# Kernel optimization log

Hardware: AMD Instinct MI355X
Metric: run time of the kernel (lower is better)

The kernel has to match this reference:

```python
import jax, jax.numpy as jnp
import numpy as np


def setup_inputs() -> dict:
    key = jax.random.key(0)
    ks = jax.random.split(key, 8)
    B, T, DIM = 4096, 64, 16
    H1, H2, LAT = 256, 256, 64
    KD = DIM + LAT  # Koopman dim = 80
    x = jax.random.normal(ks[0], (B, T, DIM), dtype=jnp.float32)
    # Encoder: Linear(16->256, bias), Linear(256->256, bias), Linear(256->64, no bias)
    W1 = jax.random.normal(ks[1], (H1, DIM), dtype=jnp.float32) / np.sqrt(DIM)
    b1 = jnp.zeros((H1,), dtype=jnp.float32)
    W2 = jax.random.normal(ks[2], (H2, H1), dtype=jnp.float32) / np.sqrt(H1)
    b2 = jnp.zeros((H2,), dtype=jnp.float32)
    W3 = jax.random.normal(ks[3], (LAT, H2), dtype=jnp.float32) / np.sqrt(H2)
    # Koopman operator, scaled for stable 63-step rollout
    K = jax.random.normal(ks[4], (KD, KD), dtype=jnp.float32) * (0.9 / np.sqrt(KD))
    return {"x": x, "W1": W1, "b1": b1, "W2": W2, "b2": b2, "W3": W3,
            "K": K, "n_shifts": 64}


def reference(x, W1, b1, W2, b2, W3, K, n_shifts):
    # x: [B, T, dim]; slice to n_shifts steps
    x = x[:, :n_shifts, :]
    # Encoder MLP (relu on all but last layer; last layer bias-free, dropout p=0)
    h = jax.nn.relu(jnp.einsum('btd,hd->bth', x, W1) + b1)
    h = jax.nn.relu(jnp.einsum('bth,gh->btg', h, W2) + b2)
    g = jnp.einsum('btg,lg->btl', h, W3)
    y = jnp.concatenate([x, g], axis=-1)  # [B, T, dim+lat]
    # Linear recurrence: y_{n+1} = y_n @ K^T, starting from y[:, 0]
    y0 = y[:, 0, :]  # [B, KD]

    def step(carry, _):
        nxt = carry @ K.T
        return nxt, nxt

    _, rest = jax.lax.scan(step, y0, None, length=n_shifts - 1)  # [T-1, B, KD]
    y_pred = jnp.concatenate([y0[:, None, :], jnp.swapaxes(rest, 0, 1)], axis=1)
    return y, y_pred
```

## Files before the change

kernel.cpp:

```cpp
#include <hip/hip_runtime.h>
#include <hip/hip_bf16.h>

#define NB   4096
#define NT   64
#define NDIM 16
#define NH1  256
#define NH2  256
#define NLAT 64
#define NKD  80
#define YROW (NT * NKD)
#define KTAB 98304
#define KSLOT 15360
#define Y0F   1081344
#define HPLANE 393216

#define FROW 184
#define FIMG_B (80 * FROW * 2)

typedef __attribute__((ext_vector_type(8))) short bf16x8;
typedef __attribute__((ext_vector_type(4))) float f32x4;

#define MFMA __builtin_amdgcn_mfma_f32_16x16x32_bf16

static __device__ __forceinline__ short f2bf(float f) {
  __hip_bfloat16 b = __float2bfloat16(f);
  return __builtin_bit_cast(short, b);
}
static __device__ __forceinline__ float bf2f(short h) {
  union { unsigned u; float f; } v; v.u = ((unsigned)(unsigned short)h) << 16;
  return v.f;
}
static __device__ __forceinline__ bf16x8 pack8(float4 a, float4 b) {
  bf16x8 r;
  r[0] = f2bf(a.x); r[1] = f2bf(a.y); r[2] = f2bf(a.z); r[3] = f2bf(a.w);
  r[4] = f2bf(b.x); r[5] = f2bf(b.y); r[6] = f2bf(b.z); r[7] = f2bf(b.w);
  return r;
}

__global__ __launch_bounds__(256) void prep_kernel(const float* __restrict__ W1,
                                                   const float* __restrict__ W2,
                                                   const float* __restrict__ W3,
                                                   short* __restrict__ ws) {
  int i = blockIdx.x * 256 + threadIdx.x;
  {
    int e = i & 7, l = (i >> 3) & 63, nt = (i >> 9) & 15, kk = i >> 13;
    int g = nt * 16 + (l & 15);
    int h = kk * 32 + (l >> 4) * 8 + e;
    ws[i] = f2bf(W2[g * NH1 + h]);
  }
  if (i < 16384) {
    int e = i & 7, l = (i >> 3) & 63, nt = (i >> 9) & 3, kk = i >> 11;
    int g = nt * 16 + (l & 15);
    int h = kk * 32 + (l >> 4) * 8 + e;
    ws[65536 + i] = f2bf(W3[g * NH2 + h]);
  }
  if (i < 8192) {
    int e = i & 7, l = (i >> 3) & 63, nt = i >> 9;
    int g = nt * 16 + (l & 15);
    int k = (l >> 4) * 8 + e;
    ws[81920 + i] = (k < NDIM) ? f2bf(W1[g * NDIM + k]) : (short)0;
  }
}

template <int XSTRIDE, int MODE>
static __device__ __forceinline__ void mlp_body(long b, const float* __restrict__ x,
                                                const float* __restrict__ b1g,
                                                const float* __restrict__ b2g,
                                                const short* __restrict__ ws,
                                                float* __restrict__ yo,
                                                short* __restrict__ y0f,
                                                short* h1s, int tid) {
  const int lane = tid & 63;
  const int w    = tid >> 6;
  const int l15  = lane & 15;
  const int kg   = lane >> 4;

  const short* W2f = ws;
  const short* W3f = ws + 65536;
  const short* W1f = ws + 81920;

  const float4 xv =
      *(const float4*)(x + (b * 64 + (tid >> 2)) * XSTRIDE + (tid & 3) * 4);

  bf16x8 xf[4];
#pragma unroll
  for (int j = 0; j < 4; ++j) {
    const int tok = j * 16 + l15;
    bf16x8 f = {};
    if (kg < 2) {
      const float4* p = (const float4*)(x + (b * 64 + tok) * XSTRIDE + kg * 8);
      f = pack8(p[0], p[1]);
    }
    xf[j] = f;
  }

#pragma unroll
  for (int i = 0; i < 4; ++i) {
    const int mt = w * 4 + i;
    const bf16x8 wa = *(const bf16x8*)(W1f + (mt * 64 + lane) * 8);
    const float4 bias = *(const float4*)(b1g + mt * 16 + kg * 4);
#pragma unroll
    for (int j = 0; j < 4; ++j) {
      f32x4 c = {0.f, 0.f, 0.f, 0.f};
      c = MFMA(wa, xf[j], c, 0, 0, 0);
      const int tok = j * 16 + l15;
      float v0 = c[0] + bias.x; v0 = v0 > 0.f ? v0 : 0.f;
      float v1 = c[1] + bias.y; v1 = v1 > 0.f ? v1 : 0.f;
      float v2 = c[2] + bias.z; v2 = v2 > 0.f ? v2 : 0.f;
      float v3 = c[3] + bias.w; v3 = v3 > 0.f ? v3 : 0.f;
      short4 st = {f2bf(v0), f2bf(v1), f2bf(v2), f2bf(v3)};
      *(short4*)(h1s + tok * 264 + mt * 16 + kg * 4) = st;
    }
  }
  __syncthreads();

  f32x4 acc2[4][4];
#pragma unroll
  for (int i = 0; i < 4; ++i)
#pragma unroll
    for (int j = 0; j < 4; ++j) acc2[i][j] = (f32x4){0.f, 0.f, 0.f, 0.f};

#pragma unroll 2
  for (int kk = 0; kk < 8; ++kk) {
    bf16x8 wa[4], hb[4];
#pragma unroll
    for (int i = 0; i < 4; ++i)
      wa[i] = *(const bf16x8*)(W2f + ((kk * 16 + w * 4 + i) * 64 + lane) * 8);
#pragma unroll
    for (int j = 0; j < 4; ++j)
      hb[j] = *(const bf16x8*)(h1s + (j * 16 + l15) * 264 + kk * 32 + kg * 8);
#pragma unroll
    for (int i = 0; i < 4; ++i)
#pragma unroll
      for (int j = 0; j < 4; ++j)
        acc2[i][j] = MFMA(wa[i], hb[j], acc2[i][j], 0, 0, 0);
  }
  __syncthreads();

#pragma unroll
  for (int i = 0; i < 4; ++i) {
    const int mt = w * 4 + i;
    const float4 bias = *(const float4*)(b2g + mt * 16 + kg * 4);
#pragma unroll
    for (int j = 0; j < 4; ++j) {
      const int tok = j * 16 + l15;
      float v0 = acc2[i][j][0] + bias.x; v0 = v0 > 0.f ? v0 : 0.f;
      float v1 = acc2[i][j][1] + bias.y; v1 = v1 > 0.f ? v1 : 0.f;
      float v2 = acc2[i][j][2] + bias.z; v2 = v2 > 0.f ? v2 : 0.f;
      float v3 = acc2[i][j][3] + bias.w; v3 = v3 > 0.f ? v3 : 0.f;
      short4 st = {f2bf(v0), f2bf(v1), f2bf(v2), f2bf(v3)};
      *(short4*)(h1s + tok * 264 + mt * 16 + kg * 4) = st;
    }
  }
  __syncthreads();

  f32x4 acc3[4];
#pragma unroll
  for (int j = 0; j < 4; ++j) acc3[j] = (f32x4){0.f, 0.f, 0.f, 0.f};
#pragma unroll 2
  for (int kk = 0; kk < 8; ++kk) {
    const bf16x8 wa = *(const bf16x8*)(W3f + ((kk * 4 + w) * 64 + lane) * 8);
#pragma unroll
    for (int j = 0; j < 4; ++j) {
      const bf16x8 hb =
          *(const bf16x8*)(h1s + (j * 16 + l15) * 264 + kk * 32 + kg * 8);
      acc3[j] = MFMA(wa, hb, acc3[j], 0, 0, 0);
    }
  }

  if (MODE == 0) {
    *(float4*)(yo + (b * 64 + (tid >> 2)) * 80 + (tid & 3) * 4) = xv;
#pragma unroll
    for (int j = 0; j < 4; ++j) {
      const int tok = j * 16 + l15;
      *(float4*)(yo + (b * 64 + tok) * 80 + 16 + w * 16 + kg * 4) =
          *(float4*)&acc3[j];
    }
  } else {
    {
      const int t0 = tid >> 2;
      const int gmt = (int)b * 4 + (t0 >> 4);
      const int c0x = (tid & 3) * 4;
      const int lanef = (c0x >> 3) * 16 + (t0 & 15);
      short h0 = f2bf(xv.x), h1 = f2bf(xv.y), h2 = f2bf(xv.z), h3 = f2bf(xv.w);
      short4 hs = {h0, h1, h2, h3};
      short4 ls = {f2bf(xv.x - bf2f(h0)), f2bf(xv.y - bf2f(h1)),
                   f2bf(xv.z - bf2f(h2)), f2bf(xv.w - bf2f(h3))};
      const int idx = ((gmt * 3 + 0) * 64 + lanef) * 8 + (c0x & 7);
      *(short4*)(y0f + idx) = hs;
      *(short4*)(y0f + HPLANE + idx) = ls;
    }
    const int c0 = 16 + w * 16 + kg * 4;
    const int kkf = c0 >> 5;
    const int lanef = ((c0 & 31) >> 3) * 16 + l15;
#pragma unroll
    for (int j = 0; j < 4; ++j) {
      const int gmt = (int)b * 4 + j;
      short h0 = f2bf(acc3[j][0]), h1 = f2bf(acc3[j][1]);
      short h2 = f2bf(acc3[j][2]), h3 = f2bf(acc3[j][3]);
      short4 hs = {h0, h1, h2, h3};
      short4 ls = {f2bf(acc3[j][0] - bf2f(h0)), f2bf(acc3[j][1] - bf2f(h1)),
                   f2bf(acc3[j][2] - bf2f(h2)), f2bf(acc3[j][3] - bf2f(h3))};
      const int idx = ((gmt * 3 + kkf) * 64 + lanef) * 8 + (c0 & 7);
      *(short4*)(y0f + idx) = hs;
      *(short4*)(y0f + HPLANE + idx) = ls;
    }
    {
      const int plane = tid & 1;
      const int lz = 32 + ((tid >> 1) & 31);
      const int gmt = (int)b * 4 + (tid >> 6);
      bf16x8 z = {};
      *(bf16x8*)(y0f + plane * HPLANE + ((gmt * 3 + 2) * 64 + lz) * 8) = z;
    }
  }
}

__global__ __launch_bounds__(256, 4) void kpow_mlp0_kernel(const float* __restrict__ Kg,
                                                           const float* __restrict__ x,
                                                           const float* __restrict__ b1g,
                                                           const float* __restrict__ b2g,
                                                           short* __restrict__ ws) {
  extern __shared__ char smem[];
  const int tid = threadIdx.x;

  if (blockIdx.x >= 63) {
    mlp_body<1024, 1>((long)(blockIdx.x - 63), x, b1g, b2g, ws, nullptr,
                      ws + Y0F, (short*)smem, tid);
    return;
  }

  short* kA   = (short*)smem;
  short* curA = (short*)(smem + FIMG_B);
  short* curB = (short*)(smem + 2 * FIMG_B);
  short* nxtA = (short*)(smem + 3 * FIMG_B);
  short* nxtB = (short*)(smem + 4 * FIMG_B);

  const int lane = tid & 63;
  const int w    = tid >> 6;
  const int l15  = lane & 15;
  const int kg   = lane >> 4;
  const int t    = blockIdx.x + 1;

  for (int i = tid; i < 6400; i += 256) {
    float v = Kg[i];
    int r = i / 80, c = i - r * 80;
    short hi = f2bf(v);
    short lo = f2bf(v - bf2f(hi));
    kA[r * FROW + c] = hi;        kA[r * FROW + 96 + c] = lo;
    curA[r * FROW + c] = hi;      curA[r * FROW + 96 + c] = lo;
    curB[c * FROW + r] = hi;      curB[c * FROW + 96 + r] = lo;
  }
  __syncthreads();

  auto mm = [&](const short* Ai, const short* Bi, short* DA, short* DB) {
    for (int id = w; id < 25; id += 4) {
      const int mt = id / 5, nt = id % 5;
      f32x4 acc = {0.f, 0.f, 0.f, 0.f};
#pragma unroll
      for (int kk = 0; kk < 3; ++kk) {
        const int k0 = kk * 32 + kg * 8;
        bf16x8 ah = {}, al = {}, bh = {}, bl = {};
        if (k0 < 80) {
          const short* ap = Ai + (mt * 16 + l15) * FROW + k0;
          const short* bp = Bi + (nt * 16 + l15) * FROW + k0;
          ah = *(const bf16x8*)ap;  al = *(const bf16x8*)(ap + 96);
          bh = *(const bf16x8*)bp;  bl = *(const bf16x8*)(bp + 96);
        }
        acc = MFMA(ah, bh, acc, 0, 0, 0);
        acc = MFMA(al, bh, acc, 0, 0, 0);
        acc = MFMA(ah, bl, acc, 0, 0, 0);
      }
      const int n = nt * 16 + l15;
      const int rowb = mt * 16 + kg * 4;
      short4 hs, ls;
#pragma unroll
      for (int r = 0; r < 4; ++r) {
        float v = acc[r];
        short hi = f2bf(v);
        short lo = f2bf(v - bf2f(hi));
        DA[(rowb + r) * FROW + n] = hi;
        DA[(rowb + r) * FROW + 96 + n] = lo;
        ((short*)&hs)[r] = hi;
        ((short*)&ls)[r] = lo;
      }
      *(short4*)(DB + n * FROW + rowb) = hs;
      *(short4*)(DB + n * FROW + 96 + rowb) = ls;
    }
    __syncthreads();
  };

  const int h = 31 - __clz(t);
  for (int bit = h - 1; bit >= 0; --bit) {
    mm(curA, curB, nxtA, nxtB);
    { short* p;
      p = curA; curA = nxtA; nxtA = p;
      p = curB; curB = nxtB; nxtB = p; }
    if ((t >> bit) & 1) {
      mm(kA, curB, nxtA, nxtB);
      { short* p;
        p = curA; curA = nxtA; nxtA = p;
        p = curB; curB = nxtB; nxtB = p; }
    }
  }

  short* kt = ws + KTAB + t * KSLOT;
  for (int s = tid; s < 960; s += 256) {
    int f = s >> 6, ln = s & 63;
    int kk = f / 5, nt = f % 5;
    int k0 = kk * 32 + (ln >> 4) * 8;
    int n  = nt * 16 + (ln & 15);
    bf16x8 h8 = {}, l8 = {};
    if (k0 < 80) {
      const short* ap = curA + n * FROW + k0;
      h8 = *(const bf16x8*)ap;
      l8 = *(const bf16x8*)(ap + 96);
    }
    *(bf16x8*)(kt + f * 512 + ln * 8) = h8;
    *(bf16x8*)(kt + 7680 + f * 512 + ln * 8) = l8;
  }
}

static __device__ __forceinline__ void ypred_body(int g, const short* __restrict__ ws,
                                                  float* __restrict__ yp, int tid) {
  const int lane = tid & 63;
  const int w    = tid >> 6;
  const int m16  = lane & 15;
  const int kg   = lane >> 4;
  const int bc   = g & 31;
  const int t    = g >> 5;
  const long b0  = (long)bc * 128;
  const short* y0f = ws + Y0F;

  if (t == 0) {
    for (int i = tid; i < 10240; i += 256) {
      const int r = i / 80, c = i - (i / 80) * 80;
      const int gmt = bc * 8 + (r >> 4);
      const int idx = ((gmt * 3 + (c >> 5)) * 64 + ((c & 31) >> 3) * 16 + (r & 15)) * 8 + (c & 7);
      yp[(b0 + r) * YROW + c] = bf2f(y0f[idx]) + bf2f(y0f[HPLANE + idx]);
    }
    return;
  }

  bf16x8 ah[2][3], al[2][3];
#pragma unroll
  for (int m = 0; m < 2; ++m) {
    const int gmt = bc * 8 + 2 * w + m;
#pragma unroll
    for (int kk = 0; kk < 3; ++kk) {
      const int idx = ((gmt * 3 + kk) * 64 + lane) * 8;
      ah[m][kk] = *(const bf16x8*)(y0f + idx);
      al[m][kk] = *(const bf16x8*)(y0f + HPLANE + idx);
    }
  }

  const short* kt = ws + KTAB + t * KSLOT;
  f32x4 acc[2][5];
#pragma unroll
  for (int m = 0; m < 2; ++m)
#pragma unroll
    for (int nt = 0; nt < 5; ++nt) acc[m][nt] = (f32x4){0.f, 0.f, 0.f, 0.f};

#pragma unroll
  for (int kk = 0; kk < 3; ++kk) {
#pragma unroll
    for (int nt = 0; nt < 5; ++nt) {
      const bf16x8 bh = *(const bf16x8*)(kt + ((kk * 5 + nt) * 64 + lane) * 8);
      const bf16x8 bl = *(const bf16x8*)(kt + 7680 + ((kk * 5 + nt) * 64 + lane) * 8);
#pragma unroll
      for (int m = 0; m < 2; ++m) {
        acc[m][nt] = MFMA(ah[m][kk], bh, acc[m][nt], 0, 0, 0);
        acc[m][nt] = MFMA(al[m][kk], bh, acc[m][nt], 0, 0, 0);
        acc[m][nt] = MFMA(ah[m][kk], bl, acc[m][nt], 0, 0, 0);
      }
    }
  }
#pragma unroll
  for (int m = 0; m < 2; ++m)
#pragma unroll
    for (int nt = 0; nt < 5; ++nt)
#pragma unroll
      for (int r = 0; r < 4; ++r)
        yp[(b0 + (2 * w + m) * 16 + kg * 4 + r) * YROW + (long)t * 80 + nt * 16 + m16] =
            acc[m][nt][r];
}

__global__ __launch_bounds__(256, 4) void fused_kernel(const float* __restrict__ x,
                                                       const float* __restrict__ b1g,
                                                       const float* __restrict__ b2g,
                                                       const short* __restrict__ ws,
                                                       float* __restrict__ y,
                                                       float* __restrict__ yp) {
  extern __shared__ char smem[];
  const int bid = blockIdx.x;
  const int g = bid / 3;
  const int r = bid - 3 * g;
  if (r == 2) {
    ypred_body(g, ws, yp, threadIdx.x);
  } else {
    mlp_body<16, 0>((long)(g * 2 + r), x, b1g, b2g, ws, y, nullptr,
                    (short*)smem, threadIdx.x);
  }
}

extern "C" void kernel_launch(void* const* d_in, const int* in_sizes, int n_in,
                              void* d_out, int out_size, void* d_ws, size_t ws_size,
                              hipStream_t stream) {
  const float* x  = (const float*)d_in[0];
  const float* W1 = (const float*)d_in[1];
  const float* b1 = (const float*)d_in[2];
  const float* W2 = (const float*)d_in[3];
  const float* b2 = (const float*)d_in[4];
  const float* W3 = (const float*)d_in[5];
  const float* Kg = (const float*)d_in[6];
  float* y  = (float*)d_out;
  float* yp = y + (long)NB * YROW;
  short* ws = (short*)d_ws;

  prep_kernel<<<256, 256, 0, stream>>>(W1, W2, W3, ws);
  kpow_mlp0_kernel<<<127, 256, 5 * FIMG_B, stream>>>(Kg, x, b1, b2, ws);
  fused_kernel<<<6144, 256, 64 * 264 * 2, stream>>>(x, b1, b2, ws, y, yp);
}
```

Measured before the change: 116.8 us.

## Split fused kernel into larger-tile MLP kernel and separate ypred kernel

Replaces the interleaved fused kernel, which ran 64-token MLP blocks alongside ypred blocks, with two launches. The first is a 512-thread MLP kernel that processes 256 tokens per block, reusing each loaded W2 fragment across 16 token tiles and prefetching the next W2 slice. The second is a standalone ypred kernel. The goal is to cut repeated weight fetches per token and raise MFMA density. The cost is an extra kernel launch, losing the overlap of MLP and ypred work, and a larger LDS footprint (about 135 KB) that may limit occupancy.

```diff
diff --git a/kernel.cpp b/kernel.cpp
--- a/kernel.cpp
+++ b/kernel.cpp
@@ -62,14 +62,12 @@
   }
 }
 
-template <int XSTRIDE, int MODE>
-static __device__ __forceinline__ void mlp_body(long b, const float* __restrict__ x,
-                                                const float* __restrict__ b1g,
-                                                const float* __restrict__ b2g,
-                                                const short* __restrict__ ws,
-                                                float* __restrict__ yo,
-                                                short* __restrict__ y0f,
-                                                short* h1s, int tid) {
+static __device__ __forceinline__ void mlp0_body(long b, const float* __restrict__ x,
+                                                 const float* __restrict__ b1g,
+                                                 const float* __restrict__ b2g,
+                                                 const short* __restrict__ ws,
+                                                 short* __restrict__ y0f,
+                                                 short* h1s, int tid) {
   const int lane = tid & 63;
   const int w    = tid >> 6;
   const int l15  = lane & 15;
@@ -80,7 +78,7 @@
   const short* W1f = ws + 81920;
 
   const float4 xv =
-      *(const float4*)(x + (b * 64 + (tid >> 2)) * XSTRIDE + (tid & 3) * 4);
+      *(const float4*)(x + (b * 64 + (tid >> 2)) * 1024 + (tid & 3) * 4);
 
   bf16x8 xf[4];
 #pragma unroll
@@ -88,7 +86,7 @@
     const int tok = j * 16 + l15;
     bf16x8 f = {};
     if (kg < 2) {
-      const float4* p = (const float4*)(x + (b * 64 + tok) * XSTRIDE + kg * 8);
+      const float4* p = (const float4*)(x + (b * 64 + tok) * 1024 + kg * 8);
       f = pack8(p[0], p[1]);
     }
     xf[j] = f;
@@ -168,50 +166,40 @@
     }
   }
 
-  if (MODE == 0) {
-    *(float4*)(yo + (b * 64 + (tid >> 2)) * 80 + (tid & 3) * 4) = xv;
-#pragma unroll
-    for (int j = 0; j < 4; ++j) {
-      const int tok = j * 16 + l15;
-      *(float4*)(yo + (b * 64 + tok) * 80 + 16 + w * 16 + kg * 4) =
-          *(float4*)&acc3[j];
-    }
-  } else {
-    {
-      const int t0 = tid >> 2;
-      const int gmt = (int)b * 4 + (t0 >> 4);
-      const int c0x = (tid & 3) * 4;
-      const int lanef = (c0x >> 3) * 16 + (t0 & 15);
-      short h0 = f2bf(xv.x), h1 = f2bf(xv.y), h2 = f2bf(xv.z), h3 = f2bf(xv.w);
-      short4 hs = {h0, h1, h2, h3};
-      short4 ls = {f2bf(xv.x - bf2f(h0)), f2bf(xv.y - bf2f(h1)),
-                   f2bf(xv.z - bf2f(h2)), f2bf(xv.w - bf2f(h3))};
-      const int idx = ((gmt * 3 + 0) * 64 + lanef) * 8 + (c0x & 7);
-      *(short4*)(y0f + idx) = hs;
-      *(short4*)(y0f + HPLANE + idx) = ls;
-    }
-    const int c0 = 16 + w * 16 + kg * 4;
-    const int kkf = c0 >> 5;
-    const int lanef = ((c0 & 31) >> 3) * 16 + l15;
-#pragma unroll
-    for (int j = 0; j < 4; ++j) {
-      const int gmt = (int)b * 4 + j;
-      short h0 = f2bf(acc3[j][0]), h1 = f2bf(acc3[j][1]);
-      short h2 = f2bf(acc3[j][2]), h3 = f2bf(acc3[j][3]);
-      short4 hs = {h0, h1, h2, h3};
-      short4 ls = {f2bf(acc3[j][0] - bf2f(h0)), f2bf(acc3[j][1] - bf2f(h1)),
-                   f2bf(acc3[j][2] - bf2f(h2)), f2bf(acc3[j][3] - bf2f(h3))};
-      const int idx = ((gmt * 3 + kkf) * 64 + lanef) * 8 + (c0 & 7);
-      *(short4*)(y0f + idx) = hs;
-      *(short4*)(y0f + HPLANE + idx) = ls;
-    }
-    {
-      const int plane = tid & 1;
-      const int lz = 32 + ((tid >> 1) & 31);
-      const int gmt = (int)b * 4 + (tid >> 6);
-      bf16x8 z = {};
-      *(bf16x8*)(y0f + plane * HPLANE + ((gmt * 3 + 2) * 64 + lz) * 8) = z;
-    }
+  {
+    const int t0 = tid >> 2;
+    const int gmt = (int)b * 4 + (t0 >> 4);
+    const int c0x = (tid & 3) * 4;
+    const int lanef = (c0x >> 3) * 16 + (t0 & 15);
+    short h0 = f2bf(xv.x), h1 = f2bf(xv.y), h2 = f2bf(xv.z), h3 = f2bf(xv.w);
+    short4 hs = {h0, h1, h2, h3};
+    short4 ls = {f2bf(xv.x - bf2f(h0)), f2bf(xv.y - bf2f(h1)),
+                 f2bf(xv.z - bf2f(h2)), f2bf(xv.w - bf2f(h3))};
+    const int idx = ((gmt * 3 + 0) * 64 + lanef) * 8 + (c0x & 7);
+    *(short4*)(y0f + idx) = hs;
+    *(short4*)(y0f + HPLANE + idx) = ls;
+  }
+  const int c0 = 16 + w * 16 + kg * 4;
+  const int kkf = c0 >> 5;
+  const int lanef = ((c0 & 31) >> 3) * 16 + l15;
+#pragma unroll
+  for (int j = 0; j < 4; ++j) {
+    const int gmt = (int)b * 4 + j;
+    short h0 = f2bf(acc3[j][0]), h1 = f2bf(acc3[j][1]);
+    short h2 = f2bf(acc3[j][2]), h3 = f2bf(acc3[j][3]);
+    short4 hs = {h0, h1, h2, h3};
+    short4 ls = {f2bf(acc3[j][0] - bf2f(h0)), f2bf(acc3[j][1] - bf2f(h1)),
+                 f2bf(acc3[j][2] - bf2f(h2)), f2bf(acc3[j][3] - bf2f(h3))};
+    const int idx = ((gmt * 3 + kkf) * 64 + lanef) * 8 + (c0 & 7);
+    *(short4*)(y0f + idx) = hs;
+    *(short4*)(y0f + HPLANE + idx) = ls;
+  }
+  {
+    const int plane = tid & 1;
+    const int lz = 32 + ((tid >> 1) & 31);
+    const int gmt = (int)b * 4 + (tid >> 6);
+    bf16x8 z = {};
+    *(bf16x8*)(y0f + plane * HPLANE + ((gmt * 3 + 2) * 64 + lz) * 8) = z;
   }
 }
 
@@ -224,8 +212,7 @@
   const int tid = threadIdx.x;
 
   if (blockIdx.x >= 63) {
-    mlp_body<1024, 1>((long)(blockIdx.x - 63), x, b1g, b2g, ws, nullptr,
-                      ws + Y0F, (short*)smem, tid);
+    mlp0_body((long)(blockIdx.x - 63), x, b1g, b2g, ws, ws + Y0F, (short*)smem, tid);
     return;
   }
 
@@ -320,14 +307,151 @@
   }
 }
 
-static __device__ __forceinline__ void ypred_body(int g, const short* __restrict__ ws,
-                                                  float* __restrict__ yp, int tid) {
+__global__ __launch_bounds__(512, 2) void mlp256_kernel(const float* __restrict__ x,
+                                                        const float* __restrict__ b1g,
+                                                        const float* __restrict__ b2g,
+                                                        const short* __restrict__ ws,
+                                                        float* __restrict__ y) {
+  extern __shared__ char smem[];
+  short* h1s = (short*)smem;
+
+  const int tid  = threadIdx.x;
+  const int lane = tid & 63;
+  const int w    = tid >> 6;
+  const int l15  = lane & 15;
+  const int kg   = lane >> 4;
+  const long b   = blockIdx.x;
+
+  const short* W2f = ws;
+  const short* W3f = ws + 65536;
+  const short* W1f = ws + 81920;
+
+#pragma unroll
+  for (int i = 0; i < 2; ++i) {
+    const int idx = i * 512 + tid;
+    const int tok = idx >> 2, c = (idx & 3) * 4;
+    const float4 v = *(const float4*)(x + (b * 256 + tok) * 16 + c);
+    *(float4*)(y + (b * 256 + tok) * 80 + c) = v;
+  }
+
+  {
+    const bf16x8 wa0 = *(const bf16x8*)(W1f + ((2 * w) * 64 + lane) * 8);
+    const bf16x8 wa1 = *(const bf16x8*)(W1f + ((2 * w + 1) * 64 + lane) * 8);
+    const float4 bias0 = *(const float4*)(b1g + (2 * w) * 16 + kg * 4);
+    const float4 bias1 = *(const float4*)(b1g + (2 * w + 1) * 16 + kg * 4);
+#pragma unroll
+    for (int nt = 0; nt < 16; ++nt) {
+      const int tok = nt * 16 + l15;
+      bf16x8 xf = {};
+      if (kg < 2) {
+        const float4* p = (const float4*)(x + (b * 256 + tok) * 16 + kg * 8);
+        xf = pack8(p[0], p[1]);
+      }
+      f32x4 c0 = {0.f, 0.f, 0.f, 0.f}, c1 = {0.f, 0.f, 0.f, 0.f};
+      c0 = MFMA(wa0, xf, c0, 0, 0, 0);
+      c1 = MFMA(wa1, xf, c1, 0, 0, 0);
+      float u0 = c0[0] + bias0.x; u0 = u0 > 0.f ? u0 : 0.f;
+      float u1 = c0[1] + bias0.y; u1 = u1 > 0.f ? u1 : 0.f;
+      float u2 = c0[2] + bias0.z; u2 = u2 > 0.f ? u2 : 0.f;
+      float u3 = c0[3] + bias0.w; u3 = u3 > 0.f ? u3 : 0.f;
+      short4 s0 = {f2bf(u0), f2bf(u1), f2bf(u2), f2bf(u3)};
+      *(short4*)(h1s + tok * 264 + (2 * w) * 16 + kg * 4) = s0;
+      float v0 = c1[0] + bias1.x; v0 = v0 > 0.f ? v0 : 0.f;
+      float v1 = c1[1] + bias1.y; v1 = v1 > 0.f ? v1 : 0.f;
+      float v2 = c1[2] + bias1.z; v2 = v2 > 0.f ? v2 : 0.f;
+      float v3 = c1[3] + bias1.w; v3 = v3 > 0.f ? v3 : 0.f;
+      short4 s1 = {f2bf(v0), f2bf(v1), f2bf(v2), f2bf(v3)};
+      *(short4*)(h1s + tok * 264 + (2 * w + 1) * 16 + kg * 4) = s1;
+    }
+  }
+  __syncthreads();
+
+  f32x4 acc2[2][16];
+#pragma unroll
+  for (int i = 0; i < 2; ++i)
+#pragma unroll
+    for (int j = 0; j < 16; ++j) acc2[i][j] = (f32x4){0.f, 0.f, 0.f, 0.f};
+
+  bf16x8 wa0 = *(const bf16x8*)(W2f + ((2 * w) * 64 + lane) * 8);
+  bf16x8 wa1 = *(const bf16x8*)(W2f + ((2 * w + 1) * 64 + lane) * 8);
+  for (int kk = 0; kk < 8; ++kk) {
+    bf16x8 nwa0, nwa1;
+    if (kk < 7) {
+      const short* wb = W2f + (((kk + 1) * 16 + 2 * w) * 64 + lane) * 8;
+      nwa0 = *(const bf16x8*)wb;
+      nwa1 = *(const bf16x8*)(wb + 512);
+    }
+#pragma unroll
+    for (int g = 0; g < 4; ++g) {
+      bf16x8 hb[4];
+#pragma unroll
+      for (int j = 0; j < 4; ++j)
+        hb[j] = *(const bf16x8*)(h1s + ((g * 4 + j) * 16 + l15) * 264 + kk * 32 + kg * 8);
+#pragma unroll
+      for (int j = 0; j < 4; ++j) {
+        acc2[0][g * 4 + j] = MFMA(wa0, hb[j], acc2[0][g * 4 + j], 0, 0, 0);
+        acc2[1][g * 4 + j] = MFMA(wa1, hb[j], acc2[1][g * 4 + j], 0, 0, 0);
+      }
+    }
+    wa0 = nwa0; wa1 = nwa1;
+  }
+  __syncthreads();
+
+  {
+    const float4 bias0 = *(const float4*)(b2g + (2 * w) * 16 + kg * 4);
+    const float4 bias1 = *(const float4*)(b2g + (2 * w + 1) * 16 + kg * 4);
+#pragma unroll
+    for (int j = 0; j < 16; ++j) {
+      const int tok = j * 16 + l15;
+      float u0 = acc2[0][j][0] + bias0.x; u0 = u0 > 0.f ? u0 : 0.f;
+      float u1 = acc2[0][j][1] + bias0.y; u1 = u1 > 0.f ? u1 : 0.f;
+      float u2 = acc2[0][j][2] + bias0.z; u2 = u2 > 0.f ? u2 : 0.f;
+      float u3 = acc2[0][j][3] + bias0.w; u3 = u3 > 0.f ? u3 : 0.f;
+      short4 s0 = {f2bf(u0), f2bf(u1), f2bf(u2), f2bf(u3)};
+      *(short4*)(h1s + tok * 264 + (2 * w) * 16 + kg * 4) = s0;
+      float v0 = acc2[1][j][0] + bias1.x; v0 = v0 > 0.f ? v0 : 0.f;
+      float v1 = acc2[1][j][1] + bias1.y; v1 = v1 > 0.f ? v1 : 0.f;
+      float v2 = acc2[1][j][2] + bias1.z; v2 = v2 > 0.f ? v2 : 0.f;
+      float v3 = acc2[1][j][3] + bias1.w; v3 = v3 > 0.f ? v3 : 0.f;
+      short4 s1 = {f2bf(v0), f2bf(v1), f2bf(v2), f2bf(v3)};
+      *(short4*)(h1s + tok * 264 + (2 * w + 1) * 16 + kg * 4) = s1;
+    }
+  }
+  __syncthreads();
+
+  const int mt3 = w & 3;
+  const int nh  = w >> 2;
+  f32x4 acc3[8];
+#pragma unroll
+  for (int j = 0; j < 8; ++j) acc3[j] = (f32x4){0.f, 0.f, 0.f, 0.f};
+#pragma unroll 2
+  for (int kk = 0; kk < 8; ++kk) {
+    const bf16x8 wa = *(const bf16x8*)(W3f + ((kk * 4 + mt3) * 64 + lane) * 8);
+#pragma unroll
+    for (int j = 0; j < 8; ++j) {
+      const bf16x8 hb =
+          *(const bf16x8*)(h1s + ((nh * 8 + j) * 16 + l15) * 264 + kk * 32 + kg * 8);
+      acc3[j] = MFMA(wa, hb, acc3[j], 0, 0, 0);
+    }
+  }
+
+#pragma unroll
+  for (int j = 0; j < 8; ++j) {
+    const int tok = (nh * 8 + j) * 16 + l15;
+    *(float4*)(y + (b * 256 + tok) * 80 + 16 + mt3 * 16 + kg * 4) =
+        *(float4*)&acc3[j];
+  }
+}
+
+__global__ __launch_bounds__(256, 4) void ypred_kernel(const short* __restrict__ ws,
+                                                       float* __restrict__ yp) {
+  const int tid  = threadIdx.x;
   const int lane = tid & 63;
   const int w    = tid >> 6;
   const int m16  = lane & 15;
   const int kg   = lane >> 4;
-  const int bc   = g & 31;
-  const int t    = g >> 5;
+  const int bc   = blockIdx.x & 31;
+  const int t    = blockIdx.x >> 5;
   const long b0  = (long)bc * 128;
   const short* y0f = ws + Y0F;
 
@@ -382,24 +506,6 @@
       for (int r = 0; r < 4; ++r)
         yp[(b0 + (2 * w + m) * 16 + kg * 4 + r) * YROW + (long)t * 80 + nt * 16 + m16] =
             acc[m][nt][r];
-}
-
-__global__ __launch_bounds__(256, 4) void fused_kernel(const float* __restrict__ x,
-                                                       const float* __restrict__ b1g,
-                                                       const float* __restrict__ b2g,
-                                                       const short* __restrict__ ws,
-                                                       float* __restrict__ y,
-                                                       float* __restrict__ yp) {
-  extern __shared__ char smem[];
-  const int bid = blockIdx.x;
-  const int g = bid / 3;
-  const int r = bid - 3 * g;
-  if (r == 2) {
-    ypred_body(g, ws, yp, threadIdx.x);
-  } else {
-    mlp_body<16, 0>((long)(g * 2 + r), x, b1g, b2g, ws, y, nullptr,
-                    (short*)smem, threadIdx.x);
-  }
 }
 
 extern "C" void kernel_launch(void* const* d_in, const int* in_sizes, int n_in,
@@ -418,5 +524,6 @@
 
   prep_kernel<<<256, 256, 0, stream>>>(W1, W2, W3, ws);
   kpow_mlp0_kernel<<<127, 256, 5 * FIMG_B, stream>>>(Kg, x, b1, b2, ws);
-  fused_kernel<<<6144, 256, 64 * 264 * 2, stream>>>(x, b1, b2, ws, y, yp);
-}
+  mlp256_kernel<<<NB / 4, 512, 256 * 264 * 2, stream>>>(x, b1, b2, ws, y);
+  ypred_kernel<<<32 * 64, 256, 0, stream>>>(ws, yp);
+}
```

Measured after the change: 170.2 us. +45.7%, slower.
